# Optimization experiments

Hardware: AMD Instinct MI355X
Metric: run time of the kernel (lower is better)

The kernel has to match this reference:

```python
import jax, jax.numpy as jnp
import numpy as np

OUT, IN = 4096, 4096          # weight_shape
VDIM = 8                      # codebook vector dim
NCODES = 4096                 # codebook entries
TOKENS = 8192


def setup_inputs() -> dict:
    key = jax.random.key(0)
    k1, k2, k3, k4, k5 = jax.random.split(key, 5)
    numel = OUT * IN
    x = jax.random.normal(k1, (TOKENS, IN), dtype=jnp.float32)
    codebook = jax.random.normal(k2, (NCODES, VDIM), dtype=jnp.float32)
    scales = jax.random.uniform(k3, (OUT, 1), dtype=jnp.float32, minval=0.5, maxval=1.5)
    indices = jax.random.randint(k4, (numel // VDIM,), 0, NCODES, dtype=jnp.int32)
    signs = jax.random.randint(k5, (numel // 8,), 0, 256, dtype=jnp.int32)  # packed bytes
    return {"x": x, "codebook": codebook, "scales": scales,
            "indices": indices, "signs": signs}


def _unpack_signs(signs):
    # big-endian bit unpack (np.packbits order): packed bytes -> {-1,+1} floats
    bits = (signs[:, None] >> jnp.arange(7, -1, -1, dtype=jnp.int32)) & 1  # [numel/8, 8]
    return (2 * bits - 1).astype(jnp.float32).reshape(OUT, IN)


def reference(x, codebook, scales, indices, signs):
    # dequant: codebook gather -> reshape -> per-row scale -> sign multiply
    w = codebook[indices].reshape(OUT, IN) * scales        # [OUT, IN]
    w = w * _unpack_signs(signs)
    # F.linear(x, w) = x @ w.T
    return jnp.einsum('ti,oi->to', x, w)
```

## Files before the change

### kernel.cpp

```cpp
#include <hip/hip_runtime.h>

#define M_ 8192
#define N_ 4096
#define K_ 4096

typedef float f32x4 __attribute__((ext_vector_type(4)));
typedef int   i32x4 __attribute__((ext_vector_type(4)));

__device__ __forceinline__ unsigned pack4(const float* v, float inv) {
  unsigned r = 0;
#pragma unroll
  for (int j = 0; j < 4; ++j) {
    int q = (int)rintf(v[j] * inv);
    q = q < -127 ? -127 : (q > 127 ? 127 : q);
    r |= ((unsigned)(q & 0xff)) << (8 * j);
  }
  return r;
}

__global__ __launch_bounds__(256) void prep_kernel(
    const float* __restrict__ x, const float* __restrict__ cb,
    const float* __restrict__ scales, const int* __restrict__ idx,
    const int* __restrict__ signs,
    signed char* __restrict__ Wq, signed char* __restrict__ Xq,
    float* __restrict__ sw, float* __restrict__ sx)
{
  __shared__ float wred[4];
  const int b = blockIdx.x, t = threadIdx.x;

  if (b < N_) {
    const float s = scales[b];
    const int g0 = b * 512 + t, g1 = g0 + 256;
    const int c0 = idx[g0], c1 = idx[g1];
    const int sb0 = signs[g0], sb1 = signs[g1];
    const float* cv0 = cb + c0 * 8;
    const float* cv1 = cb + c1 * 8;
    float v[16];
    float mx = 0.f;
#pragma unroll
    for (int j = 0; j < 8; ++j) {
      float a = cv0[j] * s;
      if (!((sb0 >> (7 - j)) & 1)) a = -a;
      v[j] = a; mx = fmaxf(mx, fabsf(a));
    }
#pragma unroll
    for (int j = 0; j < 8; ++j) {
      float a = cv1[j] * s;
      if (!((sb1 >> (7 - j)) & 1)) a = -a;
      v[8 + j] = a; mx = fmaxf(mx, fabsf(a));
    }
#pragma unroll
    for (int off = 1; off < 64; off <<= 1) mx = fmaxf(mx, __shfl_xor(mx, off));
    if ((t & 63) == 0) wred[t >> 6] = mx;
    __syncthreads();
    mx = fmaxf(fmaxf(wred[0], wred[1]), fmaxf(wred[2], wred[3]));
    mx = fmaxf(mx, 1e-20f);
    const float inv = 127.0f / mx;
    if (t == 0) sw[b] = mx / 127.0f;
    uint2 o0 = {pack4(v, inv),     pack4(v + 4, inv)};
    uint2 o1 = {pack4(v + 8, inv), pack4(v + 12, inv)};
    *(uint2*)(Wq + (size_t)b * K_ + t * 8)        = o0;
    *(uint2*)(Wq + (size_t)b * K_ + 2048 + t * 8) = o1;
  } else {
    const int r = b - N_;
    const f32x4* px = (const f32x4*)(x + (size_t)r * K_ + t * 16);
    f32x4 a0 = px[0], a1 = px[1], a2 = px[2], a3 = px[3];
    float v[16];
#pragma unroll
    for (int j = 0; j < 4; ++j) { v[j] = a0[j]; v[4 + j] = a1[j]; v[8 + j] = a2[j]; v[12 + j] = a3[j]; }
    float mx = 0.f;
#pragma unroll
    for (int j = 0; j < 16; ++j) mx = fmaxf(mx, fabsf(v[j]));
#pragma unroll
    for (int off = 1; off < 64; off <<= 1) mx = fmaxf(mx, __shfl_xor(mx, off));
    if ((t & 63) == 0) wred[t >> 6] = mx;
    __syncthreads();
    mx = fmaxf(fmaxf(wred[0], wred[1]), fmaxf(wred[2], wred[3]));
    mx = fmaxf(mx, 1e-20f);
    const float inv = 127.0f / mx;
    if (t == 0) sx[r] = mx / 127.0f;
    uint4 o = {pack4(v, inv), pack4(v + 4, inv), pack4(v + 8, inv), pack4(v + 12, inv)};
    *(uint4*)(Xq + (size_t)r * K_ + t * 16) = o;
  }
}

#define BM 256
#define BN 256
#define BK 64
#define NT (K_ / BK)

#define GLDS(g, l) __builtin_amdgcn_global_load_lds( \
    (const __attribute__((address_space(1))) void*)(g), \
    (__attribute__((address_space(3))) void*)(l), 16, 0, 0)

#define LGKM0 do { \
    asm volatile("s_waitcnt lgkmcnt(0)" ::: "memory"); \
    __builtin_amdgcn_sched_barrier(0); \
  } while (0)

#define VM_WAIT(n) asm volatile("s_waitcnt vmcnt(" #n ")" ::: "memory")
#define MEMFENCE asm volatile("" ::: "memory")

template<int MODE>
__device__ __forceinline__ void tile_step(
    int T, signed char (*lds)[2][16384], i32x4 (&acc)[8][4],
    const signed char* __restrict__ Ag,
    const signed char* __restrict__ Bg,
    int wm, int wn, int lrow, int cs16,
    int tid, int sr, int scs)
{
  const int b = T & 1, nb = b ^ 1;
  i32x4 av[4], bv[4];

#pragma unroll
  for (int m = 0; m < 4; ++m)
    av[m] = *(const i32x4*)(const void*)(
        &lds[b][0][(wm * 128 + m * 16 + lrow) * 64 + cs16]);
#pragma unroll
  for (int n = 0; n < 4; ++n)
    bv[n] = *(const i32x4*)(const void*)(
        &lds[b][1][(wn * 64 + n * 16 + lrow) * 64 + cs16]);
  if (MODE <= 1) {
    GLDS(Ag + (size_t)(sr) * K_ + (T + 1) * BK + scs,       &lds[nb][0][tid * 16]);
    GLDS(Ag + (size_t)(128 + sr) * K_ + (T + 1) * BK + scs, &lds[nb][0][8192 + tid * 16]);
  }
  __builtin_amdgcn_s_barrier();
  LGKM0;
  __builtin_amdgcn_s_setprio(1);
#pragma unroll
  for (int n = 0; n < 4; ++n)
#pragma unroll
    for (int m = 0; m < 4; ++m)
      acc[m][n] = __builtin_amdgcn_mfma_i32_16x16x64_i8(av[m], bv[n], acc[m][n], 0, 0, 0);
  __builtin_amdgcn_s_setprio(0);
  __builtin_amdgcn_s_barrier();
  MEMFENCE;

#pragma unroll
  for (int m = 0; m < 4; ++m)
    av[m] = *(const i32x4*)(const void*)(
        &lds[b][0][(wm * 128 + 64 + m * 16 + lrow) * 64 + cs16]);
  if (MODE == 0) {
    GLDS(Bg + (size_t)(sr) * K_ + (T + 2) * BK + scs,       &lds[b][1][tid * 16]);
    GLDS(Bg + (size_t)(128 + sr) * K_ + (T + 2) * BK + scs, &lds[b][1][8192 + tid * 16]);
  }
  __builtin_amdgcn_s_barrier();
  LGKM0;
  __builtin_amdgcn_s_setprio(1);
#pragma unroll
  for (int n = 0; n < 4; ++n)
#pragma unroll
    for (int m = 0; m < 4; ++m)
      acc[4 + m][n] = __builtin_amdgcn_mfma_i32_16x16x64_i8(av[m], bv[n], acc[4 + m][n], 0, 0, 0);
  __builtin_amdgcn_s_setprio(0);
  if (MODE == 0)      VM_WAIT(2);
  else if (MODE == 1) VM_WAIT(0);
  __builtin_amdgcn_s_barrier();
  MEMFENCE;
}

__global__ __launch_bounds__(512, 2) void gemmq_kernel(
    const signed char* __restrict__ A,
    const signed char* __restrict__ B,
    const float* __restrict__ sx, const float* __restrict__ sw,
    float* __restrict__ C)
{
  __shared__ signed char lds[2][2][16384];

  const int nwg = (M_ / BM) * (N_ / BN);
  const int bid = blockIdx.x;
  const int wg  = (bid % 8) * (nwg / 8) + bid / 8;
  const int tn  = wg % (N_ / BN);
  const int tm  = wg / (N_ / BN);
  const int brow = tm * BM, bcol = tn * BN;

  const int tid  = threadIdx.x;
  const int lane = tid & 63, w = tid >> 6;
  const int wm   = w >> 2, wn = w & 3;
  const int lrow = lane & 15, hi2 = lane >> 4;
  const int cs16 = (hi2 ^ ((lrow >> 1) & 3)) * 16;
  const int sr  = tid >> 2;
  const int scs = ((tid & 3) ^ ((tid >> 3) & 3)) * 16;

  const signed char* Ag = A + (size_t)brow * K_;
  const signed char* Bg = B + (size_t)bcol * K_;

  i32x4 acc[8][4];
#pragma unroll
  for (int m = 0; m < 8; ++m)
#pragma unroll
    for (int n = 0; n < 4; ++n)
      acc[m][n] = i32x4{0, 0, 0, 0};

  GLDS(Ag + (size_t)(sr) * K_ + scs,            &lds[0][0][tid * 16]);
  GLDS(Ag + (size_t)(128 + sr) * K_ + scs,      &lds[0][0][8192 + tid * 16]);
  GLDS(Bg + (size_t)(sr) * K_ + scs,            &lds[0][1][tid * 16]);
  GLDS(Bg + (size_t)(128 + sr) * K_ + scs,      &lds[0][1][8192 + tid * 16]);
  GLDS(Bg + (size_t)(sr) * K_ + BK + scs,       &lds[1][1][tid * 16]);
  GLDS(Bg + (size_t)(128 + sr) * K_ + BK + scs, &lds[1][1][8192 + tid * 16]);
  VM_WAIT(2);
  __builtin_amdgcn_s_barrier();
  MEMFENCE;

  for (int T = 0; T < NT - 2; ++T)
    tile_step<0>(T, lds, acc, Ag, Bg, wm, wn, lrow, cs16, tid, sr, scs);
  tile_step<1>(NT - 2, lds, acc, Ag, Bg, wm, wn, lrow, cs16, tid, sr, scs);
  tile_step<2>(NT - 1, lds, acc, Ag, Bg, wm, wn, lrow, cs16, tid, sr, scs);

  const int crow = brow + wm * 128 + hi2 * 4;
  const int ccol = bcol + wn * 64 + lrow;
  float swv[4];
#pragma unroll
  for (int n = 0; n < 4; ++n) swv[n] = sw[ccol + n * 16];
#pragma unroll
  for (int m = 0; m < 8; ++m)
#pragma unroll
    for (int r = 0; r < 4; ++r) {
      const int row = crow + m * 16 + r;
      const float sxv = sx[row];
#pragma unroll
      for (int n = 0; n < 4; ++n)
        C[(size_t)row * N_ + ccol + n * 16] = (float)acc[m][n][r] * sxv * swv[n];
    }
}

__global__ __launch_bounds__(256) void fallback_kernel(
    const float* __restrict__ x, const float* __restrict__ cb,
    const float* __restrict__ scales, const int* __restrict__ idx,
    const int* __restrict__ signs, float* __restrict__ out)
{
  __shared__ float Xs[32][33];
  __shared__ float Ws[32][33];
  const int t = threadIdx.x;
  const int tx = t & 31, ty = t >> 5;
  const int brow = blockIdx.y * 32, bcol = blockIdx.x * 32;
  float acc[4] = {0.f, 0.f, 0.f, 0.f};

  for (int k0 = 0; k0 < K_; k0 += 32) {
    for (int l = t; l < 1024; l += 256) {
      const int r = l >> 5, c = l & 31;
      Xs[r][c] = x[(size_t)(brow + r) * K_ + k0 + c];
      const int n = bcol + r;
      const size_t flat = (size_t)n * K_ + (k0 + c);
      const int g = (int)(flat >> 3), j = (int)(flat & 7);
      float wv = cb[idx[g] * 8 + j] * scales[n];
      if (!((signs[g] >> (7 - j)) & 1)) wv = -wv;
      Ws[r][c] = wv;
    }
    __syncthreads();
#pragma unroll
    for (int kk = 0; kk < 32; ++kk) {
      const float wv = Ws[tx][kk];
      acc[0] += Xs[ty][kk] * wv;
      acc[1] += Xs[ty + 8][kk] * wv;
      acc[2] += Xs[ty + 16][kk] * wv;
      acc[3] += Xs[ty + 24][kk] * wv;
    }
    __syncthreads();
  }
#pragma unroll
  for (int q = 0; q < 4; ++q)
    out[(size_t)(brow + ty + 8 * q) * N_ + bcol + tx] = acc[q];
}

extern "C" void kernel_launch(void* const* d_in, const int* in_sizes, int n_in,
                              void* d_out, int out_size, void* d_ws, size_t ws_size,
                              hipStream_t stream)
{
  const float* x      = (const float*)d_in[0];
  const float* cb     = (const float*)d_in[1];
  const float* scales = (const float*)d_in[2];
  const int*   idx    = (const int*)d_in[3];
  const int*   signs  = (const int*)d_in[4];
  float* out = (float*)d_out;

  const size_t wq = (size_t)N_ * K_;
  const size_t xq = (size_t)M_ * K_;
  const size_t need = wq + xq + (N_ + M_) * sizeof(float);

  if (ws_size >= need) {
    signed char* Wq = (signed char*)d_ws;
    signed char* Xq = Wq + wq;
    float* swp = (float*)(Xq + xq);
    float* sxp = swp + N_;
    prep_kernel<<<N_ + M_, 256, 0, stream>>>(x, cb, scales, idx, signs, Wq, Xq, swp, sxp);
    gemmq_kernel<<<(M_ / BM) * (N_ / BN), 512, 0, stream>>>(Xq, Wq, sxp, swp, out);
  } else {
    fallback_kernel<<<dim3(N_ / 32, M_ / 32), 256, 0, stream>>>(x, cb, scales, idx, signs, out);
  }
}
```

Before: 186.7 us.

## Prefetch next-tile LDS fragments across steps and halve barriers per K-step

Restructures the int8 GEMM main loop so the A/B register fragments for the next K-tile are read from LDS at the end of the current step, instead of at its start. The second A half is loaded at the start of the step and overlaps the first MFMA block through a partial lgkmcnt wait. Barriers per step drop from four to two, cutting sync stalls and exposed LDS latency. The cost is extra live fragment registers, which could pressure VGPRs at occupancy 2, plus more delicate buffer-reuse ordering.

```diff
diff --git a/kernel.cpp b/kernel.cpp
--- a/kernel.cpp
+++ b/kernel.cpp
@@ -93,8 +93,8 @@
     (const __attribute__((address_space(1))) void*)(g), \
     (__attribute__((address_space(3))) void*)(l), 16, 0, 0)
 
-#define LGKM0 do { \
-    asm volatile("s_waitcnt lgkmcnt(0)" ::: "memory"); \
+#define LGKM_WAIT(n) do { \
+    asm volatile("s_waitcnt lgkmcnt(" #n ")" ::: "memory"); \
     __builtin_amdgcn_sched_barrier(0); \
   } while (0)
 
@@ -104,59 +104,63 @@
 template<int MODE>
 __device__ __forceinline__ void tile_step(
     int T, signed char (*lds)[2][16384], i32x4 (&acc)[8][4],
+    i32x4 (&av0)[4], i32x4 (&av1)[4], i32x4 (&bv)[4],
     const signed char* __restrict__ Ag,
     const signed char* __restrict__ Bg,
     int wm, int wn, int lrow, int cs16,
     int tid, int sr, int scs)
 {
   const int b = T & 1, nb = b ^ 1;
-  i32x4 av[4], bv[4];
 
 #pragma unroll
   for (int m = 0; m < 4; ++m)
-    av[m] = *(const i32x4*)(const void*)(
-        &lds[b][0][(wm * 128 + m * 16 + lrow) * 64 + cs16]);
-#pragma unroll
-  for (int n = 0; n < 4; ++n)
-    bv[n] = *(const i32x4*)(const void*)(
-        &lds[b][1][(wn * 64 + n * 16 + lrow) * 64 + cs16]);
+    av1[m] = *(const i32x4*)(const void*)(
+        &lds[b][0][(wm * 128 + 64 + m * 16 + lrow) * 64 + cs16]);
   if (MODE <= 1) {
     GLDS(Ag + (size_t)(sr) * K_ + (T + 1) * BK + scs,       &lds[nb][0][tid * 16]);
     GLDS(Ag + (size_t)(128 + sr) * K_ + (T + 1) * BK + scs, &lds[nb][0][8192 + tid * 16]);
   }
-  __builtin_amdgcn_s_barrier();
-  LGKM0;
+
+  LGKM_WAIT(4);
   __builtin_amdgcn_s_setprio(1);
 #pragma unroll
   for (int n = 0; n < 4; ++n)
 #pragma unroll
     for (int m = 0; m < 4; ++m)
-      acc[m][n] = __builtin_amdgcn_mfma_i32_16x16x64_i8(av[m], bv[n], acc[m][n], 0, 0, 0);
+      acc[m][n] = __builtin_amdgcn_mfma_i32_16x16x64_i8(av0[m], bv[n], acc[m][n], 0, 0, 0);
   __builtin_amdgcn_s_setprio(0);
+
+  LGKM_WAIT(0);
+  __builtin_amdgcn_s_setprio(1);
+#pragma unroll
+  for (int n = 0; n < 4; ++n)
+#pragma unroll
+    for (int m = 0; m < 4; ++m)
+      acc[4 + m][n] = __builtin_amdgcn_mfma_i32_16x16x64_i8(av1[m], bv[n], acc[4 + m][n], 0, 0, 0);
+  __builtin_amdgcn_s_setprio(0);
+
+  if (MODE == 2) return;
+
   __builtin_amdgcn_s_barrier();
   MEMFENCE;
-
-#pragma unroll
-  for (int m = 0; m < 4; ++m)
-    av[m] = *(const i32x4*)(const void*)(
-        &lds[b][0][(wm * 128 + 64 + m * 16 + lrow) * 64 + cs16]);
   if (MODE == 0) {
     GLDS(Bg + (size_t)(sr) * K_ + (T + 2) * BK + scs,       &lds[b][1][tid * 16]);
     GLDS(Bg + (size_t)(128 + sr) * K_ + (T + 2) * BK + scs, &lds[b][1][8192 + tid * 16]);
-  }
-  __builtin_amdgcn_s_barrier();
-  LGKM0;
-  __builtin_amdgcn_s_setprio(1);
-#pragma unroll
-  for (int n = 0; n < 4; ++n)
-#pragma unroll
-    for (int m = 0; m < 4; ++m)
-      acc[4 + m][n] = __builtin_amdgcn_mfma_i32_16x16x64_i8(av[m], bv[n], acc[4 + m][n], 0, 0, 0);
-  __builtin_amdgcn_s_setprio(0);
-  if (MODE == 0)      VM_WAIT(2);
-  else if (MODE == 1) VM_WAIT(0);
+    VM_WAIT(2);
+  } else {
+    VM_WAIT(0);
+  }
   __builtin_amdgcn_s_barrier();
   MEMFENCE;
+
+#pragma unroll
+  for (int m = 0; m < 4; ++m)
+    av0[m] = *(const i32x4*)(const void*)(
+        &lds[nb][0][(wm * 128 + m * 16 + lrow) * 64 + cs16]);
+#pragma unroll
+  for (int n = 0; n < 4; ++n)
+    bv[n] = *(const i32x4*)(const void*)(
+        &lds[nb][1][(wn * 64 + n * 16 + lrow) * 64 + cs16]);
 }
 
 __global__ __launch_bounds__(512, 2) void gemmq_kernel(
@@ -202,10 +206,20 @@
   __builtin_amdgcn_s_barrier();
   MEMFENCE;
 
+  i32x4 av0[4], av1[4], bv[4];
+#pragma unroll
+  for (int m = 0; m < 4; ++m)
+    av0[m] = *(const i32x4*)(const void*)(
+        &lds[0][0][(wm * 128 + m * 16 + lrow) * 64 + cs16]);
+#pragma unroll
+  for (int n = 0; n < 4; ++n)
+    bv[n] = *(const i32x4*)(const void*)(
+        &lds[0][1][(wn * 64 + n * 16 + lrow) * 64 + cs16]);
+
   for (int T = 0; T < NT - 2; ++T)
-    tile_step<0>(T, lds, acc, Ag, Bg, wm, wn, lrow, cs16, tid, sr, scs);
-  tile_step<1>(NT - 2, lds, acc, Ag, Bg, wm, wn, lrow, cs16, tid, sr, scs);
-  tile_step<2>(NT - 1, lds, acc, Ag, Bg, wm, wn, lrow, cs16, tid, sr, scs);
+    tile_step<0>(T, lds, acc, av0, av1, bv, Ag, Bg, wm, wn, lrow, cs16, tid, sr, scs);
+  tile_step<1>(NT - 2, lds, acc, av0, av1, bv, Ag, Bg, wm, wn, lrow, cs16, tid, sr, scs);
+  tile_step<2>(NT - 1, lds, acc, av0, av1, bv, Ag, Bg, wm, wn, lrow, cs16, tid, sr, scs);
 
   const int crow = brow + wm * 128 + hi2 * 4;
   const int ccol = bcol + wn * 64 + lrow;
```

New measurement: 187.5 us. About the same (+0.4%).
